# Kernel optimization log

Measured on AMD Instinct MI355X. Metric: run time of the kernel, lower is better.

## Reference

```python
import jax, jax.numpy as jnp
import numpy as np

STATE_DIM = 1024
INPUT_DIM = 1024
BATCH = 8192


def setup_inputs() -> dict:
    key = jax.random.key(0)
    ks = jax.random.split(key, 7)
    # Kaiming-uniform-ish init like torch Linear
    bx = 1.0 / np.sqrt(INPUT_DIM)
    bh = 1.0 / np.sqrt(STATE_DIM)
    return {
        "x": jax.random.normal(ks[0], (BATCH, INPUT_DIM), jnp.float32),
        "prevh": jax.random.normal(ks[1], (BATCH, STATE_DIM), jnp.float32),
        "prevc": jax.random.normal(ks[2], (BATCH, STATE_DIM), jnp.float32),
        "Wx": jax.random.uniform(ks[3], (INPUT_DIM, 4 * STATE_DIM), jnp.float32, -bx, bx),
        "bx": jax.random.uniform(ks[4], (4 * STATE_DIM,), jnp.float32, -bx, bx),
        "Wh": jax.random.uniform(ks[5], (STATE_DIM, 4 * STATE_DIM), jnp.float32, -bh, bh),
    }


def reference(x, prevh, prevc, Wx, bx, Wh):
    # stacked gate pre-activations: [B, 4*state_dim]
    stacked = x @ Wx + bx + prevh @ Wh
    i_bar, f_bar, o_bar, g_bar = jnp.split(stacked, 4, axis=1)
    i = jax.nn.sigmoid(i_bar)
    f = jax.nn.sigmoid(f_bar)
    o = jax.nn.sigmoid(o_bar)
    g = jnp.tanh(g_bar)
    nextc = prevc * f + g * i
    nexth = jnp.tanh(nextc) * o
    return (nexth, nextc)
```

## Files before the change

kernel.cpp:

```cpp
#include <hip/hip_runtime.h>
#include <hip/hip_bf16.h>


#define BATCH   8192
#define SDIM    1024
#define KDIM    2048
#define NDIM    4096

typedef __attribute__((ext_vector_type(8))) short s16x8;
typedef __attribute__((ext_vector_type(4))) float f32x4;

__device__ __forceinline__ void gload16(const void* g, void* l) {
    __builtin_amdgcn_global_load_lds((const __attribute__((address_space(1))) void*)g,
                                     (__attribute__((address_space(3))) void*)l,
                                     16, 0, 0);
}

__device__ __forceinline__ float fast_sigmoid(float x) {
    return 1.0f / (1.0f + __expf(-x));
}
__device__ __forceinline__ float fast_tanh(float v) {
    float a = fabsf(v);
    float e = __expf(-2.0f * a);
    float t = (1.0f - e) / (1.0f + e);
    return copysignf(t, v);
}

__global__ void convA(const float* __restrict__ x, const float* __restrict__ h,
                      __hip_bfloat16* __restrict__ A) {
    int t = blockIdx.x * blockDim.x + threadIdx.x;
    int e = t << 3;
    int b = e >> 11;
    int k = e & 2047;
    const float* src = (k < 1024) ? (x + (size_t)b * 1024 + k)
                                  : (h + (size_t)b * 1024 + (k - 1024));
    float4 v0 = *(const float4*)(src);
    float4 v1 = *(const float4*)(src + 4);
    union { __hip_bfloat16 b[8]; s16x8 v; } u;
    u.b[0] = __float2bfloat16(v0.x); u.b[1] = __float2bfloat16(v0.y);
    u.b[2] = __float2bfloat16(v0.z); u.b[3] = __float2bfloat16(v0.w);
    u.b[4] = __float2bfloat16(v1.x); u.b[5] = __float2bfloat16(v1.y);
    u.b[6] = __float2bfloat16(v1.z); u.b[7] = __float2bfloat16(v1.w);
    *(s16x8*)(A + e) = u.v;
}

__global__ void convW(const float* __restrict__ Wx, const float* __restrict__ Wh,
                      __hip_bfloat16* __restrict__ Wt) {
    __shared__ float tile[32][33];
    int k0 = blockIdx.x * 32;
    int n0 = blockIdx.y * 32;
    int tx = threadIdx.x;
    int ty = threadIdx.y;
#pragma unroll
    for (int j = 0; j < 4; ++j) {
        int k = k0 + ty + j * 8;
        int n = n0 + tx;
        float v = (k < 1024) ? Wx[(size_t)k * 4096 + n]
                             : Wh[(size_t)(k - 1024) * 4096 + n];
        tile[ty + j * 8][tx] = v;
    }
    __syncthreads();
#pragma unroll
    for (int j = 0; j < 4; ++j) {
        int n = n0 + ty + j * 8;
        int k = k0 + tx;
        Wt[(size_t)n * 2048 + k] = __float2bfloat16(tile[tx][ty + j * 8]);
    }
}

__global__ __launch_bounds__(256, 2) void lstm_gemm(
    const __hip_bfloat16* __restrict__ A,
    const __hip_bfloat16* __restrict__ Wt,
    const float* __restrict__ bx,
    const float* __restrict__ prevc,
    float* __restrict__ outh,
    float* __restrict__ outc)
{
    __shared__ __align__(16) __hip_bfloat16 ldsA[128 * 64];
    __shared__ __align__(16) __hip_bfloat16 ldsB[128 * 64];

    const int tid  = threadIdx.x;
    const int lane = tid & 63;
    const int w    = tid >> 6;
    const int wr   = w >> 1;
    const int wc   = w & 1;
    const int m0   = blockIdx.x * 128;
    const int s0   = blockIdx.y * 32;

    f32x4 acc[4][4];
#pragma unroll
    for (int m = 0; m < 4; ++m)
#pragma unroll
        for (int g = 0; g < 4; ++g)
            acc[m][g] = (f32x4)0.0f;

    const int srow = lane >> 3;
    const int skof = (lane & 7) * 8;
    const __hip_bfloat16* Ag = A + (size_t)m0 * KDIM;

    for (int kt = 0; kt < KDIM; kt += 64) {
#pragma unroll
        for (int c = 0; c < 4; ++c) {
            int r = c * 32 + w * 8 + srow;
            gload16(Ag + (size_t)r * KDIM + kt + skof, &ldsA[c * 2048 + w * 512]);
        }
#pragma unroll
        for (int c = 0; c < 4; ++c) {
            int gs   = c * 32 + w * 8 + srow;
            int gate = gs >> 5;
            int sof  = gs & 31;
            gload16(Wt + (size_t)(gate * 1024 + s0 + sof) * KDIM + kt + skof,
                    &ldsB[c * 2048 + w * 512]);
        }
        __syncthreads();

        s16x8 af[4][2], bf[4][2];
#pragma unroll
        for (int m = 0; m < 4; ++m)
#pragma unroll
            for (int kf = 0; kf < 2; ++kf)
                af[m][kf] = *(const s16x8*)&ldsA[(wr * 64 + m * 16 + (lane & 15)) * 64
                                                 + kf * 32 + (lane >> 4) * 8];
#pragma unroll
        for (int g = 0; g < 4; ++g)
#pragma unroll
            for (int kf = 0; kf < 2; ++kf)
                bf[g][kf] = *(const s16x8*)&ldsB[(g * 32 + wc * 16 + (lane & 15)) * 64
                                                 + kf * 32 + (lane >> 4) * 8];
#pragma unroll
        for (int kf = 0; kf < 2; ++kf)
#pragma unroll
            for (int m = 0; m < 4; ++m)
#pragma unroll
                for (int g = 0; g < 4; ++g)
                    acc[m][g] = __builtin_amdgcn_mfma_f32_16x16x32_bf16(
                        af[m][kf], bf[g][kf], acc[m][g], 0, 0, 0);
        __syncthreads();
    }

    const int scol = s0 + wc * 16 + (lane & 15);
    const float b_i = bx[scol];
    const float b_f = bx[1024 + scol];
    const float b_o = bx[2048 + scol];
    const float b_g = bx[3072 + scol];
    const int rbase = m0 + wr * 64 + (lane >> 4) * 4;

#pragma unroll
    for (int m = 0; m < 4; ++m) {
#pragma unroll
        for (int q = 0; q < 4; ++q) {
            int row = rbase + m * 16 + q;
            float ib = acc[m][0][q] + b_i;
            float fb = acc[m][1][q] + b_f;
            float ob = acc[m][2][q] + b_o;
            float gb = acc[m][3][q] + b_g;
            float ig = fast_sigmoid(ib);
            float fg = fast_sigmoid(fb);
            float og = fast_sigmoid(ob);
            float gg = fast_tanh(gb);
            float pc = prevc[(size_t)row * SDIM + scol];
            float nc = pc * fg + gg * ig;
            float nh = fast_tanh(nc) * og;
            outh[(size_t)row * SDIM + scol] = nh;
            outc[(size_t)row * SDIM + scol] = nc;
        }
    }
}

extern "C" void kernel_launch(void* const* d_in, const int* in_sizes, int n_in,
                              void* d_out, int out_size, void* d_ws, size_t ws_size,
                              hipStream_t stream) {
    const float* x     = (const float*)d_in[0];
    const float* prevh = (const float*)d_in[1];
    const float* prevc = (const float*)d_in[2];
    const float* Wx    = (const float*)d_in[3];
    const float* bx    = (const float*)d_in[4];
    const float* Wh    = (const float*)d_in[5];

    __hip_bfloat16* Abf = (__hip_bfloat16*)d_ws;
    __hip_bfloat16* Wt  = Abf + (size_t)BATCH * KDIM;

    float* outh = (float*)d_out;
    float* outc = outh + (size_t)BATCH * SDIM;

    hipLaunchKernelGGL(convA, dim3(8192), dim3(256), 0, stream, x, prevh, Abf);
    hipLaunchKernelGGL(convW, dim3(64, 128), dim3(32, 8), 0, stream, Wx, Wh, Wt);
    hipLaunchKernelGGL(lstm_gemm, dim3(64, 32), dim3(256), 0, stream,
                       Abf, Wt, bx, prevc, outh, outc);
}
```

Before: 179.5 us.

## Enlarge GEMM tiles to 256x256 with 4-stage async LDS pipeline and swizzle

Reworks the fused LSTM GEMM to use 256x256 output tiles with 512 threads and a 4-deep ring of LDS buffers filled by async global-to-LDS loads. The k-step is 32, synchronisation uses explicit vmcnt waits instead of double __syncthreads, and LDS reads use an XOR swizzle to avoid bank conflicts. The weight-transpose kernel now permutes gate rows so each 256-column tile holds all four gates for 64 states, and block IDs are swizzled to improve L2 reuse. The aim is more MFMA work per byte loaded and latency hidden by prefetching. The cost is 128KB of LDS per block and more accumulator registers, which may reduce occupancy below the 2 blocks requested in the launch bounds.

```diff
diff --git a/kernel.cpp b/kernel.cpp
--- a/kernel.cpp
+++ b/kernel.cpp
@@ -5,7 +5,7 @@
 #define BATCH   8192
 #define SDIM    1024
 #define KDIM    2048
-#define NDIM    4096
+#define NT      64
 
 typedef __attribute__((ext_vector_type(8))) short s16x8;
 typedef __attribute__((ext_vector_type(4))) float f32x4;
@@ -64,11 +64,12 @@
     for (int j = 0; j < 4; ++j) {
         int n = n0 + ty + j * 8;
         int k = k0 + tx;
-        Wt[(size_t)n * 2048 + k] = __float2bfloat16(tile[tx][ty + j * 8]);
-    }
-}
-
-__global__ __launch_bounds__(256, 2) void lstm_gemm(
+        int np = ((n & 1023) >> 4) * 64 + (n >> 10) * 16 + (n & 15);
+        Wt[(size_t)np * 2048 + k] = __float2bfloat16(tile[tx][ty + j * 8]);
+    }
+}
+
+__global__ __launch_bounds__(512, 2) void lstm_gemm(
     const __hip_bfloat16* __restrict__ A,
     const __hip_bfloat16* __restrict__ Wt,
     const float* __restrict__ bx,
@@ -76,77 +77,97 @@
     float* __restrict__ outh,
     float* __restrict__ outc)
 {
-    __shared__ __align__(16) __hip_bfloat16 ldsA[128 * 64];
-    __shared__ __align__(16) __hip_bfloat16 ldsB[128 * 64];
+    __shared__ __align__(16) __hip_bfloat16 lds[4 * 16384];
 
     const int tid  = threadIdx.x;
     const int lane = tid & 63;
     const int w    = tid >> 6;
-    const int wr   = w >> 1;
-    const int wc   = w & 1;
-    const int m0   = blockIdx.x * 128;
-    const int s0   = blockIdx.y * 32;
-
-    f32x4 acc[4][4];
-#pragma unroll
-    for (int m = 0; m < 4; ++m)
+    const int wr   = w >> 2;
+    const int wc   = w & 3;
+
+    const int bid = blockIdx.x;
+    const int swz = (bid & 7) * 64 + (bid >> 3);
+    const int m0  = (swz & 31) * 256;
+    const int nt  = swz >> 5;
+    const int n0  = nt * 256;
+    const int S0  = nt * 64;
+
+    f32x4 acc[8][4];
+#pragma unroll
+    for (int m = 0; m < 8; ++m)
 #pragma unroll
         for (int g = 0; g < 4; ++g)
             acc[m][g] = (f32x4)0.0f;
 
-    const int srow = lane >> 3;
-    const int skof = (lane & 7) * 8;
-    const __hip_bfloat16* Ag = A + (size_t)m0 * KDIM;
-
-    for (int kt = 0; kt < KDIM; kt += 64) {
-#pragma unroll
-        for (int c = 0; c < 4; ++c) {
-            int r = c * 32 + w * 8 + srow;
-            gload16(Ag + (size_t)r * KDIM + kt + skof, &ldsA[c * 2048 + w * 512]);
-        }
-#pragma unroll
-        for (int c = 0; c < 4; ++c) {
-            int gs   = c * 32 + w * 8 + srow;
-            int gate = gs >> 5;
-            int sof  = gs & 31;
-            gload16(Wt + (size_t)(gate * 1024 + s0 + sof) * KDIM + kt + skof,
-                    &ldsB[c * 2048 + w * 512]);
-        }
-        __syncthreads();
-
-        s16x8 af[4][2], bf[4][2];
-#pragma unroll
-        for (int m = 0; m < 4; ++m)
-#pragma unroll
-            for (int kf = 0; kf < 2; ++kf)
-                af[m][kf] = *(const s16x8*)&ldsA[(wr * 64 + m * 16 + (lane & 15)) * 64
-                                                 + kf * 32 + (lane >> 4) * 8];
+    const int srow = lane >> 2;
+    const int scol = (((lane & 3) ^ ((lane >> 2) & 3)) << 3);
+    const __hip_bfloat16* Ag = A  + (size_t)m0 * KDIM;
+    const __hip_bfloat16* Bg = Wt + (size_t)n0 * KDIM;
+
+    auto STAGE = [&](int t) {
+        const int b  = (t & 3) * 16384;
+        const int kt = t * 32;
+#pragma unroll
+        for (int r = 0; r < 2; ++r) {
+            int row = r * 128 + w * 16 + srow;
+            gload16(Ag + (size_t)row * KDIM + kt + scol,
+                    &lds[b + r * 4096 + w * 512]);
+        }
+#pragma unroll
+        for (int r = 0; r < 2; ++r) {
+            int row = r * 128 + w * 16 + srow;
+            gload16(Bg + (size_t)row * KDIM + kt + scol,
+                    &lds[b + 8192 + r * 4096 + w * 512]);
+        }
+    };
+
+    STAGE(0);
+    STAGE(1);
+
+    const int sslot = (((lane >> 4) ^ (lane & 3)) << 4);
+    const int arow  = wr * 128 + (lane & 15);
+    const int brow  = wc * 64  + (lane & 15);
+
+    for (int t = 0; t < NT; ++t) {
+        if (t + 2 < NT) {
+            STAGE(t + 2);
+            asm volatile("s_waitcnt vmcnt(8)" ::: "memory");
+        } else if (t + 1 < NT) {
+            asm volatile("s_waitcnt vmcnt(4)" ::: "memory");
+        } else {
+            asm volatile("s_waitcnt vmcnt(0)" ::: "memory");
+        }
+        __builtin_amdgcn_s_barrier();
+        __builtin_amdgcn_sched_barrier(0);
+
+        const char* base = (const char*)lds + (t & 3) * 32768;
+        s16x8 af[8], bfr[4];
+#pragma unroll
+        for (int m = 0; m < 8; ++m)
+            af[m] = *(const s16x8*)(base + (arow + m * 16) * 64 + sslot);
 #pragma unroll
         for (int g = 0; g < 4; ++g)
-#pragma unroll
-            for (int kf = 0; kf < 2; ++kf)
-                bf[g][kf] = *(const s16x8*)&ldsB[(g * 32 + wc * 16 + (lane & 15)) * 64
-                                                 + kf * 32 + (lane >> 4) * 8];
-#pragma unroll
-        for (int kf = 0; kf < 2; ++kf)
-#pragma unroll
-            for (int m = 0; m < 4; ++m)
-#pragma unroll
-                for (int g = 0; g < 4; ++g)
-                    acc[m][g] = __builtin_amdgcn_mfma_f32_16x16x32_bf16(
-                        af[m][kf], bf[g][kf], acc[m][g], 0, 0, 0);
-        __syncthreads();
-    }
-
-    const int scol = s0 + wc * 16 + (lane & 15);
-    const float b_i = bx[scol];
-    const float b_f = bx[1024 + scol];
-    const float b_o = bx[2048 + scol];
-    const float b_g = bx[3072 + scol];
-    const int rbase = m0 + wr * 64 + (lane >> 4) * 4;
-
-#pragma unroll
-    for (int m = 0; m < 4; ++m) {
+            bfr[g] = *(const s16x8*)(base + 16384 + (brow + g * 16) * 64 + sslot);
+
+        __builtin_amdgcn_s_setprio(1);
+#pragma unroll
+        for (int m = 0; m < 8; ++m)
+#pragma unroll
+            for (int g = 0; g < 4; ++g)
+                acc[m][g] = __builtin_amdgcn_mfma_f32_16x16x32_bf16(
+                    af[m], bfr[g], acc[m][g], 0, 0, 0);
+        __builtin_amdgcn_s_setprio(0);
+    }
+
+    const int st  = S0 + wc * 16 + (lane & 15);
+    const float b_i = bx[st];
+    const float b_f = bx[1024 + st];
+    const float b_o = bx[2048 + st];
+    const float b_g = bx[3072 + st];
+    const int rbase = m0 + wr * 128 + (lane >> 4) * 4;
+
+#pragma unroll
+    for (int m = 0; m < 8; ++m) {
 #pragma unroll
         for (int q = 0; q < 4; ++q) {
             int row = rbase + m * 16 + q;
@@ -158,11 +179,11 @@
             float fg = fast_sigmoid(fb);
             float og = fast_sigmoid(ob);
             float gg = fast_tanh(gb);
-            float pc = prevc[(size_t)row * SDIM + scol];
+            float pc = prevc[(size_t)row * SDIM + st];
             float nc = pc * fg + gg * ig;
             float nh = fast_tanh(nc) * og;
-            outh[(size_t)row * SDIM + scol] = nh;
-            outc[(size_t)row * SDIM + scol] = nc;
+            outh[(size_t)row * SDIM + st] = nh;
+            outc[(size_t)row * SDIM + st] = nc;
         }
     }
 }
@@ -185,6 +206,6 @@
 
     hipLaunchKernelGGL(convA, dim3(8192), dim3(256), 0, stream, x, prevh, Abf);
     hipLaunchKernelGGL(convW, dim3(64, 128), dim3(32, 8), 0, stream, Wx, Wh, Wt);
-    hipLaunchKernelGGL(lstm_gemm, dim3(64, 32), dim3(256), 0, stream,
+    hipLaunchKernelGGL(lstm_gemm, dim3(512), dim3(512), 0, stream,
                        Abf, Wt, bx, prevc, outh, outc);
 }
```

Measured after the change: 175.0 us. -2.5%, faster.
